# Kernel tuning notes

Measured on AMD Instinct MI355X. Metric: run time of the kernel, lower is better.

Reference implementation:

```python
import jax, jax.numpy as jnp
import numpy as np

B = 16384        # batch
P = 8            # num policies (experts)
D = 512          # latent dim
A = 64           # action dim
H = 1024         # hidden dim


def setup_inputs() -> dict:
    key = jax.random.key(0)
    ks = jax.random.split(key, 7)
    latents = jax.random.normal(ks[0], (B, D), dtype=jnp.float32)
    actions = jax.random.normal(ks[1], (B, A), dtype=jnp.float32)
    policy_indices = jax.random.randint(ks[2], (B,), 0, P, dtype=jnp.int64)
    # Per-policy 2-layer MLP params: concat(latent, action) -> hidden -> latent
    scale1 = 1.0 / np.sqrt(D + A)
    scale2 = 1.0 / np.sqrt(H)
    W1 = jax.random.normal(ks[3], (P, D + A, H), dtype=jnp.float32) * scale1
    b1 = jnp.zeros((P, H), dtype=jnp.float32)
    W2 = jax.random.normal(ks[4], (P, H, D), dtype=jnp.float32) * scale2
    b2 = jnp.zeros((P, D), dtype=jnp.float32)
    return {"latents": latents, "actions": actions, "policy_indices": policy_indices,
            "W1": W1, "b1": b1, "W2": W2, "b2": b2}


def reference(latents, actions, policy_indices, W1, b1, W2, b2):
    # Original: for each policy i, route rows with policy_indices == i through
    # that policy's dynamics model; scatter results back into next_latents.
    # Equivalent dense form: run all experts, then select per-row expert output.
    x = jnp.concatenate([latents, actions], axis=-1)          # [B, D+A]
    h = jax.nn.relu(jnp.einsum('bd,pdh->bph', x, W1) + b1)    # [B, P, H]
    y = jnp.einsum('bph,phd->bpd', h, W2) + b2                # [B, P, D]
    idx = policy_indices[:, None, None]                       # [B, 1, 1]
    next_latents = jnp.take_along_axis(y, idx, axis=1)[:, 0]  # [B, D]
    return next_latents
```

## Files before the change

kernel.cpp:

```cpp
#include <hip/hip_runtime.h>
#include <hip/hip_bf16.h>
#include <stdint.h>
#include <utility>

#define B_SZ 16384
#define P_SZ 8
#define D_SZ 512
#define A_SZ 64
#define K1 576
#define H_SZ 1024
#define NSEG 64
#define MB_MAX 264
#define BPAD (B_SZ + P_SZ*64)
#define PREP_BLOCKS (BPAD * 72 / 256)
#define TRANS_BLOCKS (32 * 32 * 16)

#define WAIT_VM8  0x0F78
#define WAIT_VM0  0x0F70

typedef __bf16 bf16_t;
typedef __bf16 bf16x8 __attribute__((ext_vector_type(8)));
typedef float f32x4 __attribute__((ext_vector_type(4)));

__device__ __forceinline__ void glds16(const void* g, void* l) {
    __builtin_amdgcn_global_load_lds(
        (const __attribute__((address_space(1))) unsigned*)g,
        (__attribute__((address_space(3))) unsigned*)l, 16, 0, 0);
}

template <int... Ks, typename F>
__device__ __forceinline__ void static_for_impl(std::integer_sequence<int, Ks...>, F&& f) {
    (f(std::integral_constant<int, Ks>{}), ...);
}
template <int N, typename F>
__device__ __forceinline__ void static_for(F&& f) {
    static_for_impl(std::make_integer_sequence<int, N>{}, (F&&)f);
}


__global__ __launch_bounds__(256) void hist_block(const int* __restrict__ pol,
                                                  int* __restrict__ blockhist,
                                                  int* __restrict__ rowidx) {
    __shared__ int lc[P_SZ];
    int t = threadIdx.x;
    if (t < P_SZ) lc[t] = 0;
    __syncthreads();
    int gid = blockIdx.x * 256 + t;
    rowidx[gid] = -1;
    if (gid < BPAD - B_SZ) rowidx[B_SZ + gid] = -1;
    atomicAdd(&lc[pol[gid]], 1);
    __syncthreads();
    if (t < P_SZ) blockhist[blockIdx.x * P_SZ + t] = lc[t];
}

__global__ __launch_bounds__(64) void prefix_kernel(const int* __restrict__ blockhist,
                                                    int* __restrict__ counts,
                                                    int* __restrict__ cursors,
                                                    int* __restrict__ blk_p) {
    int t = threadIdx.x;
    if (t < P_SZ) {
        int s = 0;
        for (int b = 0; b < NSEG; ++b) s += blockhist[b * P_SZ + t];
        counts[t] = s;
    }
    __syncthreads();
    if (t == 0) {
        int run = 0;
        for (int p = 0; p < P_SZ; ++p) {
            cursors[p] = run;
            int nb = (counts[p] + 63) >> 6;
            for (int b = 0; b < nb; ++b) blk_p[(run >> 6) + b] = p;
            run += nb * 64;
        }
        for (int b = run >> 6; b < MB_MAX; ++b) blk_p[b] = -1;
    }
}

__global__ __launch_bounds__(256) void scatter_agg(const int* __restrict__ pol,
                                                   int* __restrict__ cursors,
                                                   int* __restrict__ rowidx) {
    __shared__ int lc[P_SZ], base_s[P_SZ];
    int t = threadIdx.x;
    if (t < P_SZ) lc[t] = 0;
    __syncthreads();
    int i = blockIdx.x * 256 + t;
    int p = pol[i];
    int lpos = atomicAdd(&lc[p], 1);
    __syncthreads();
    if (t < P_SZ) base_s[t] = atomicAdd(&cursors[t], lc[t]);
    __syncthreads();
    rowidx[base_s[p] + lpos] = i;
}


__global__ __launch_bounds__(256) void prep_all(const float* __restrict__ latents,
                                                const float* __restrict__ actions,
                                                const int* __restrict__ rowidx,
                                                const float* __restrict__ W1,
                                                const float* __restrict__ W2,
                                                bf16_t* __restrict__ xs,
                                                bf16_t* __restrict__ w1t,
                                                bf16_t* __restrict__ w2t) {
    int bx = blockIdx.x;
    int tid = threadIdx.x;
    if (bx < PREP_BLOCKS) {
        int idx = bx * 256 + tid;
        int s = idx / 72;
        int col = (idx - s * 72) * 8;
        int g = rowidx[s];
        bf16x8 o;
        if (g < 0) {
            o = (bf16x8){0,0,0,0,0,0,0,0};
        } else {
            const float* src;
            if (col < D_SZ) src = latents + (size_t)g * D_SZ + col;
            else            src = actions + (size_t)g * A_SZ + (col - D_SZ);
            f32x4 v0 = *(const f32x4*)src;
            f32x4 v1 = *(const f32x4*)(src + 4);
            o[0] = (bf16_t)v0[0]; o[1] = (bf16_t)v0[1]; o[2] = (bf16_t)v0[2]; o[3] = (bf16_t)v0[3];
            o[4] = (bf16_t)v1[0]; o[5] = (bf16_t)v1[1]; o[6] = (bf16_t)v1[2]; o[7] = (bf16_t)v1[3];
        }
        *(bf16x8*)(xs + (size_t)s * K1 + col) = o;
        return;
    }
    int tz = bx - PREP_BLOCKS;
    int z = tz >> 10;
    int rem = tz & 1023;
    int k0 = (rem & 31) * 32, n0 = (rem >> 5) * 32;
    int K = (z < P_SZ) ? K1 : H_SZ;
    int N = (z < P_SZ) ? H_SZ : D_SZ;
    if (k0 >= K || n0 >= N) return;
    int p = z & 7;
    const float* Wp = ((z < P_SZ) ? W1 : W2) + (size_t)p * K * N;
    bf16_t* WTp = ((z < P_SZ) ? w1t : w2t) + (size_t)p * N * K;
    __shared__ float ls[32][33];
#pragma unroll
    for (int e = 0; e < 4; ++e) {
        int idx = e * 256 + tid;
        int kk = idx >> 5, nn = idx & 31;
        ls[kk][nn] = Wp[(size_t)(k0 + kk) * N + n0 + nn];
    }
    __syncthreads();
#pragma unroll
    for (int e = 0; e < 2; ++e) {
        int idx = e * 256 + tid;
        int nn = idx >> 4, kp = (idx & 15) * 2;
        union { bf16_t h[2]; unsigned u; } pk;
        pk.h[0] = (bf16_t)ls[kp][nn];
        pk.h[1] = (bf16_t)ls[kp + 1][nn];
        *(unsigned*)&WTp[(size_t)(n0 + nn) * K + k0 + kp] = pk.u;
    }
}


__global__ __launch_bounds__(64) void gemm1_kernel(
    const bf16_t* __restrict__ xs, const bf16_t* __restrict__ w1t,
    const float* __restrict__ b1, const int* __restrict__ blk_p,
    bf16_t* __restrict__ h) {

    const int p = blk_p[blockIdx.x];
    if (p < 0) return;
    const int m0 = blockIdx.x * 64;
    const int n0 = blockIdx.y * 64;

    __shared__ __align__(16) bf16_t As[3][64 * 32];
    __shared__ __align__(16) bf16_t Bs[3][64 * 32];

    const int lane = threadIdx.x;
    const bf16_t* a_src[4];
    const bf16_t* b_src[4];
    int dstc[4];
#pragma unroll
    for (int i = 0; i < 4; ++i) {
        int c = i * 64 + lane;
        int r = c >> 2;
        int kl = (c & 3) ^ ((r >> 1) & 3);
        a_src[i] = xs + (size_t)(m0 + r) * K1 + kl * 8;
        b_src[i] = w1t + ((size_t)p * H_SZ + n0 + r) * K1 + kl * 8;
        dstc[i] = c * 8;
    }

    const int l16 = lane & 15, qd = lane >> 4;
    const int swz = (l16 >> 1) & 3;
    int aoff[4], boff[4];
#pragma unroll
    for (int i = 0; i < 4; ++i) aoff[i] = (i * 16 + l16) * 32 + ((qd ^ swz) * 8);
#pragma unroll
    for (int j = 0; j < 4; ++j) boff[j] = (j * 16 + l16) * 32 + ((qd ^ swz) * 8);

    f32x4 acc[4][4];
#pragma unroll
    for (int i = 0; i < 4; ++i)
#pragma unroll
        for (int j = 0; j < 4; ++j)
            acc[i][j] = (f32x4){0.f, 0.f, 0.f, 0.f};

    constexpr int NK = K1 / 32;
#pragma unroll
    for (int i = 0; i < 4; ++i) glds16(a_src[i], &As[0][dstc[i]]);
#pragma unroll
    for (int i = 0; i < 4; ++i) glds16(b_src[i], &Bs[0][dstc[i]]);
#pragma unroll
    for (int i = 0; i < 4; ++i) glds16(a_src[i] + 32, &As[1][dstc[i]]);
#pragma unroll
    for (int i = 0; i < 4; ++i) glds16(b_src[i] + 32, &Bs[1][dstc[i]]);

    static_for<NK>([&](auto kc) {
        constexpr int k = kc.value;
        constexpr int cur = k % 3;
        if constexpr (k == NK - 1) __builtin_amdgcn_s_waitcnt(WAIT_VM0);
        else                       __builtin_amdgcn_s_waitcnt(WAIT_VM8);
        __builtin_amdgcn_sched_barrier(0);
        bf16x8 af[4], bfv[4];
#pragma unroll
        for (int i = 0; i < 4; ++i) af[i] = *(const bf16x8*)(&As[cur][aoff[i]]);
#pragma unroll
        for (int j = 0; j < 4; ++j) bfv[j] = *(const bf16x8*)(&Bs[cur][boff[j]]);
        if constexpr (k + 2 < NK) {
            constexpr int nxt = (k + 2) % 3;
#pragma unroll
            for (int i = 0; i < 4; ++i) glds16(a_src[i] + (k + 2) * 32, &As[nxt][dstc[i]]);
#pragma unroll
            for (int i = 0; i < 4; ++i) glds16(b_src[i] + (k + 2) * 32, &Bs[nxt][dstc[i]]);
        }
#pragma unroll
        for (int i = 0; i < 4; ++i)
#pragma unroll
            for (int j = 0; j < 4; ++j)
                acc[i][j] = __builtin_amdgcn_mfma_f32_16x16x32_bf16(af[i], bfv[j], acc[i][j], 0, 0, 0);
    });

#pragma unroll
    for (int i = 0; i < 4; ++i) {
#pragma unroll
        for (int r = 0; r < 4; ++r) {
            int ml = i * 16 + qd * 4 + r;
            size_t row = (size_t)(m0 + ml);
#pragma unroll
            for (int j = 0; j < 4; ++j) {
                int n = n0 + j * 16 + l16;
                float v = acc[i][j][r] + b1[p * H_SZ + n];
                h[row * H_SZ + n] = (bf16_t)fmaxf(v, 0.f);
            }
        }
    }
}

__global__ __launch_bounds__(64) void gemm2_kernel(
    const bf16_t* __restrict__ h, const bf16_t* __restrict__ w2t,
    const float* __restrict__ b2, const int* __restrict__ blk_p,
    const int* __restrict__ rowidx, float* __restrict__ out) {

    const int p = blk_p[blockIdx.x];
    if (p < 0) return;
    const int m0 = blockIdx.x * 64;
    const int n0 = blockIdx.y * 64;

    __shared__ __align__(16) bf16_t As[3][64 * 32];
    __shared__ __align__(16) bf16_t Bs[3][64 * 32];

    const int lane = threadIdx.x;
    const bf16_t* a_src[4];
    const bf16_t* b_src[4];
    int dstc[4];
#pragma unroll
    for (int i = 0; i < 4; ++i) {
        int c = i * 64 + lane;
        int r = c >> 2;
        int kl = (c & 3) ^ ((r >> 1) & 3);
        a_src[i] = h + (size_t)(m0 + r) * H_SZ + kl * 8;
        b_src[i] = w2t + ((size_t)p * D_SZ + n0 + r) * H_SZ + kl * 8;
        dstc[i] = c * 8;
    }

    const int l16 = lane & 15, qd = lane >> 4;
    const int swz = (l16 >> 1) & 3;
    int aoff[4], boff[4];
#pragma unroll
    for (int i = 0; i < 4; ++i) aoff[i] = (i * 16 + l16) * 32 + ((qd ^ swz) * 8);
#pragma unroll
    for (int j = 0; j < 4; ++j) boff[j] = (j * 16 + l16) * 32 + ((qd ^ swz) * 8);

    f32x4 acc[4][4];
#pragma unroll
    for (int i = 0; i < 4; ++i)
#pragma unroll
        for (int j = 0; j < 4; ++j)
            acc[i][j] = (f32x4){0.f, 0.f, 0.f, 0.f};

    constexpr int NK = H_SZ / 32;
#pragma unroll
    for (int i = 0; i < 4; ++i) glds16(a_src[i], &As[0][dstc[i]]);
#pragma unroll
    for (int i = 0; i < 4; ++i) glds16(b_src[i], &Bs[0][dstc[i]]);
#pragma unroll
    for (int i = 0; i < 4; ++i) glds16(a_src[i] + 32, &As[1][dstc[i]]);
#pragma unroll
    for (int i = 0; i < 4; ++i) glds16(b_src[i] + 32, &Bs[1][dstc[i]]);

    static_for<NK>([&](auto kc) {
        constexpr int k = kc.value;
        constexpr int cur = k % 3;
        if constexpr (k == NK - 1) __builtin_amdgcn_s_waitcnt(WAIT_VM0);
        else                       __builtin_amdgcn_s_waitcnt(WAIT_VM8);
        __builtin_amdgcn_sched_barrier(0);
        bf16x8 af[4], bfv[4];
#pragma unroll
        for (int i = 0; i < 4; ++i) af[i] = *(const bf16x8*)(&As[cur][aoff[i]]);
#pragma unroll
        for (int j = 0; j < 4; ++j) bfv[j] = *(const bf16x8*)(&Bs[cur][boff[j]]);
        if constexpr (k + 2 < NK) {
            constexpr int nxt = (k + 2) % 3;
#pragma unroll
            for (int i = 0; i < 4; ++i) glds16(a_src[i] + (k + 2) * 32, &As[nxt][dstc[i]]);
#pragma unroll
            for (int i = 0; i < 4; ++i) glds16(b_src[i] + (k + 2) * 32, &Bs[nxt][dstc[i]]);
        }
#pragma unroll
        for (int i = 0; i < 4; ++i)
#pragma unroll
            for (int j = 0; j < 4; ++j)
                acc[i][j] = __builtin_amdgcn_mfma_f32_16x16x32_bf16(af[i], bfv[j], acc[i][j], 0, 0, 0);
    });

#pragma unroll
    for (int i = 0; i < 4; ++i) {
#pragma unroll
        for (int r = 0; r < 4; ++r) {
            int ml = i * 16 + qd * 4 + r;
            int g = rowidx[m0 + ml];
            if (g >= 0) {
                size_t orow = (size_t)g * D_SZ;
#pragma unroll
                for (int j = 0; j < 4; ++j) {
                    int n = n0 + j * 16 + l16;
                    out[orow + n] = acc[i][j][r] + b2[p * D_SZ + n];
                }
            }
        }
    }
}


extern "C" void kernel_launch(void* const* d_in, const int* in_sizes, int n_in,
                              void* d_out, int out_size, void* d_ws, size_t ws_size,
                              hipStream_t stream) {
    const float* latents = (const float*)d_in[0];
    const float* actions = (const float*)d_in[1];
    const int*   pol     = (const int*)d_in[2];
    const float* W1      = (const float*)d_in[3];
    const float* b1      = (const float*)d_in[4];
    const float* W2      = (const float*)d_in[5];
    const float* b2      = (const float*)d_in[6];
    float* out = (float*)d_out;

    char* ws = (char*)d_ws;
    int* counts    = (int*)ws;
    int* cursors   = counts + P_SZ;
    int* blk_p     = cursors + P_SZ;
    int* blockhist = blk_p + MB_MAX;
    int* rowidx    = blockhist + NSEG * P_SZ;
    size_t pos = ((size_t)(2 * P_SZ + MB_MAX + NSEG * P_SZ + BPAD) * sizeof(int) + 255) & ~(size_t)255;
    bf16_t* xs  = (bf16_t*)(ws + pos);  pos += (size_t)BPAD * K1 * 2;
    bf16_t* hbuf= (bf16_t*)(ws + pos);  pos += (size_t)BPAD * H_SZ * 2;
    bf16_t* w1t = (bf16_t*)(ws + pos);  pos += (size_t)P_SZ * H_SZ * K1 * 2;
    bf16_t* w2t = (bf16_t*)(ws + pos);  pos += (size_t)P_SZ * D_SZ * H_SZ * 2;

    hist_block<<<NSEG, 256, 0, stream>>>(pol, blockhist, rowidx);
    prefix_kernel<<<1, 64, 0, stream>>>(blockhist, counts, cursors, blk_p);
    scatter_agg<<<NSEG, 256, 0, stream>>>(pol, cursors, rowidx);
    prep_all<<<PREP_BLOCKS + TRANS_BLOCKS, 256, 0, stream>>>(
        latents, actions, rowidx, W1, W2, xs, w1t, w2t);
    gemm1_kernel<<<dim3(MB_MAX, H_SZ / 64), 64, 0, stream>>>(xs, w1t, b1, blk_p, hbuf);
    gemm2_kernel<<<dim3(MB_MAX, D_SZ / 64), 64, 0, stream>>>(hbuf, w2t, b2, blk_p, rowidx, out);
}
```

Before: 238.1 us.

## Use 256-thread blocks with larger 256-row tiles in grouped GEMMs

Both expert GEMM kernels move from single-wave 64x64 tiles to four-wave blocks with 256-row M tiles (256x128 for the first GEMM, 256x64 for the second). Per-expert padding changes from 64 to 256 rows, and the block map and workspace sizes change to match. The goal is more reuse of each weight tile across rows and fewer blocks. In exchange, the triple-buffered async-load pipeline is replaced by a single buffer guarded by two barriers per K step, so loads no longer overlap compute, and more padded rows are computed.

Result: faster. 210.5 us (-11.6%).

```diff
diff --git a/kernel.cpp b/kernel.cpp
--- a/kernel.cpp
+++ b/kernel.cpp
@@ -1,7 +1,6 @@
 #include <hip/hip_runtime.h>
 #include <hip/hip_bf16.h>
 #include <stdint.h>
-#include <utility>
 
 #define B_SZ 16384
 #define P_SZ 8
@@ -10,13 +9,10 @@
 #define K1 576
 #define H_SZ 1024
 #define NSEG 64
-#define MB_MAX 264
-#define BPAD (B_SZ + P_SZ*64)
+#define MB_MAX 72
+#define BPAD (B_SZ + P_SZ*256)
 #define PREP_BLOCKS (BPAD * 72 / 256)
 #define TRANS_BLOCKS (32 * 32 * 16)
-
-#define WAIT_VM8  0x0F78
-#define WAIT_VM0  0x0F70
 
 typedef __bf16 bf16_t;
 typedef __bf16 bf16x8 __attribute__((ext_vector_type(8)));
@@ -26,15 +22,6 @@
     __builtin_amdgcn_global_load_lds(
         (const __attribute__((address_space(1))) unsigned*)g,
         (__attribute__((address_space(3))) unsigned*)l, 16, 0, 0);
-}
-
-template <int... Ks, typename F>
-__device__ __forceinline__ void static_for_impl(std::integer_sequence<int, Ks...>, F&& f) {
-    (f(std::integral_constant<int, Ks>{}), ...);
-}
-template <int N, typename F>
-__device__ __forceinline__ void static_for(F&& f) {
-    static_for_impl(std::make_integer_sequence<int, N>{}, (F&&)f);
 }
 
 
@@ -68,11 +55,11 @@
         int run = 0;
         for (int p = 0; p < P_SZ; ++p) {
             cursors[p] = run;
-            int nb = (counts[p] + 63) >> 6;
-            for (int b = 0; b < nb; ++b) blk_p[(run >> 6) + b] = p;
-            run += nb * 64;
+            int nb = (counts[p] + 255) >> 8;
+            for (int b = 0; b < nb; ++b) blk_p[(run >> 8) + b] = p;
+            run += nb * 256;
         }
-        for (int b = run >> 6; b < MB_MAX; ++b) blk_p[b] = -1;
+        for (int b = run >> 8; b < MB_MAX; ++b) blk_p[b] = -1;
     }
 }
 
@@ -153,91 +140,83 @@
 }
 
 
-__global__ __launch_bounds__(64) void gemm1_kernel(
+__global__ __launch_bounds__(256, 2) void gemm1_kernel(
     const bf16_t* __restrict__ xs, const bf16_t* __restrict__ w1t,
     const float* __restrict__ b1, const int* __restrict__ blk_p,
     bf16_t* __restrict__ h) {
 
     const int p = blk_p[blockIdx.x];
     if (p < 0) return;
-    const int m0 = blockIdx.x * 64;
-    const int n0 = blockIdx.y * 64;
-
-    __shared__ __align__(16) bf16_t As[3][64 * 32];
-    __shared__ __align__(16) bf16_t Bs[3][64 * 32];
-
-    const int lane = threadIdx.x;
-    const bf16_t* a_src[4];
-    const bf16_t* b_src[4];
-    int dstc[4];
+    const int m0 = blockIdx.x * 256;
+    const int n0 = blockIdx.y * 128;
+
+    __shared__ __align__(16) bf16_t As[256 * 32];
+    __shared__ __align__(16) bf16_t Bs[128 * 32];
+
+    const int tid = threadIdx.x;
+    const int wave = tid >> 6, lane = tid & 63;
+
+    const bf16_t* a_src[4]; bf16_t* a_dst[4];
 #pragma unroll
     for (int i = 0; i < 4; ++i) {
-        int c = i * 64 + lane;
+        int c = (wave * 4 + i) * 64 + lane;
         int r = c >> 2;
         int kl = (c & 3) ^ ((r >> 1) & 3);
         a_src[i] = xs + (size_t)(m0 + r) * K1 + kl * 8;
+        a_dst[i] = As + c * 8;
+    }
+    const bf16_t* b_src[2]; bf16_t* b_dst[2];
+#pragma unroll
+    for (int i = 0; i < 2; ++i) {
+        int c = (wave * 2 + i) * 64 + lane;
+        int r = c >> 2;
+        int kl = (c & 3) ^ ((r >> 1) & 3);
         b_src[i] = w1t + ((size_t)p * H_SZ + n0 + r) * K1 + kl * 8;
-        dstc[i] = c * 8;
+        b_dst[i] = Bs + c * 8;
     }
 
     const int l16 = lane & 15, qd = lane >> 4;
     const int swz = (l16 >> 1) & 3;
-    int aoff[4], boff[4];
-#pragma unroll
-    for (int i = 0; i < 4; ++i) aoff[i] = (i * 16 + l16) * 32 + ((qd ^ swz) * 8);
-#pragma unroll
-    for (int j = 0; j < 4; ++j) boff[j] = (j * 16 + l16) * 32 + ((qd ^ swz) * 8);
-
-    f32x4 acc[4][4];
+    int aoff[4], boff[8];
+#pragma unroll
+    for (int i = 0; i < 4; ++i) aoff[i] = (wave * 64 + i * 16 + l16) * 32 + ((qd ^ swz) * 8);
+#pragma unroll
+    for (int j = 0; j < 8; ++j) boff[j] = (j * 16 + l16) * 32 + ((qd ^ swz) * 8);
+
+    f32x4 acc[4][8];
 #pragma unroll
     for (int i = 0; i < 4; ++i)
 #pragma unroll
-        for (int j = 0; j < 4; ++j)
+        for (int j = 0; j < 8; ++j)
             acc[i][j] = (f32x4){0.f, 0.f, 0.f, 0.f};
 
-    constexpr int NK = K1 / 32;
-#pragma unroll
-    for (int i = 0; i < 4; ++i) glds16(a_src[i], &As[0][dstc[i]]);
-#pragma unroll
-    for (int i = 0; i < 4; ++i) glds16(b_src[i], &Bs[0][dstc[i]]);
-#pragma unroll
-    for (int i = 0; i < 4; ++i) glds16(a_src[i] + 32, &As[1][dstc[i]]);
-#pragma unroll
-    for (int i = 0; i < 4; ++i) glds16(b_src[i] + 32, &Bs[1][dstc[i]]);
-
-    static_for<NK>([&](auto kc) {
-        constexpr int k = kc.value;
-        constexpr int cur = k % 3;
-        if constexpr (k == NK - 1) __builtin_amdgcn_s_waitcnt(WAIT_VM0);
-        else                       __builtin_amdgcn_s_waitcnt(WAIT_VM8);
-        __builtin_amdgcn_sched_barrier(0);
-        bf16x8 af[4], bfv[4];
-#pragma unroll
-        for (int i = 0; i < 4; ++i) af[i] = *(const bf16x8*)(&As[cur][aoff[i]]);
-#pragma unroll
-        for (int j = 0; j < 4; ++j) bfv[j] = *(const bf16x8*)(&Bs[cur][boff[j]]);
-        if constexpr (k + 2 < NK) {
-            constexpr int nxt = (k + 2) % 3;
-#pragma unroll
-            for (int i = 0; i < 4; ++i) glds16(a_src[i] + (k + 2) * 32, &As[nxt][dstc[i]]);
-#pragma unroll
-            for (int i = 0; i < 4; ++i) glds16(b_src[i] + (k + 2) * 32, &Bs[nxt][dstc[i]]);
-        }
+    for (int kt = 0; kt < K1; kt += 32) {
+        __syncthreads();
+#pragma unroll
+        for (int i = 0; i < 4; ++i) glds16(a_src[i] + kt, a_dst[i]);
+#pragma unroll
+        for (int i = 0; i < 2; ++i) glds16(b_src[i] + kt, b_dst[i]);
+        __syncthreads();
+        bf16x8 af[4], bfv[8];
+#pragma unroll
+        for (int i = 0; i < 4; ++i) af[i] = *(const bf16x8*)(As + aoff[i]);
+#pragma unroll
+        for (int j = 0; j < 8; ++j) bfv[j] = *(const bf16x8*)(Bs + boff[j]);
 #pragma unroll
         for (int i = 0; i < 4; ++i)
 #pragma unroll
-            for (int j = 0; j < 4; ++j)
+            for (int j = 0; j < 8; ++j)
                 acc[i][j] = __builtin_amdgcn_mfma_f32_16x16x32_bf16(af[i], bfv[j], acc[i][j], 0, 0, 0);
-    });
+    }
 
 #pragma unroll
     for (int i = 0; i < 4; ++i) {
 #pragma unroll
         for (int r = 0; r < 4; ++r) {
-            int ml = i * 16 + qd * 4 + r;
+            int ml = wave * 64 + i * 16 + qd * 4 + r;
             size_t row = (size_t)(m0 + ml);
 #pragma unroll
-            for (int j = 0; j < 4; ++j) {
+            for (int j = 0; j < 8; ++j) {
                 int n = n0 + j * 16 + l16;
                 float v = acc[i][j][r] + b1[p * H_SZ + n];
                 h[row * H_SZ + n] = (bf16_t)fmaxf(v, 0.f);
@@ -246,38 +225,45 @@
     }
 }
 
-__global__ __launch_bounds__(64) void gemm2_kernel(
+__global__ __launch_bounds__(256, 2) void gemm2_kernel(
     const bf16_t* __restrict__ h, const bf16_t* __restrict__ w2t,
     const float* __restrict__ b2, const int* __restrict__ blk_p,
     const int* __restrict__ rowidx, float* __restrict__ out) {
 
     const int p = blk_p[blockIdx.x];
     if (p < 0) return;
-    const int m0 = blockIdx.x * 64;
+    const int m0 = blockIdx.x * 256;
     const int n0 = blockIdx.y * 64;
 
-    __shared__ __align__(16) bf16_t As[3][64 * 32];
-    __shared__ __align__(16) bf16_t Bs[3][64 * 32];
-
-    const int lane = threadIdx.x;
-    const bf16_t* a_src[4];
-    const bf16_t* b_src[4];
-    int dstc[4];
+    __shared__ __align__(16) bf16_t As[256 * 32];
+    __shared__ __align__(16) bf16_t Bs[64 * 32];
+
+    const int tid = threadIdx.x;
+    const int wave = tid >> 6, lane = tid & 63;
+
+    const bf16_t* a_src[4]; bf16_t* a_dst[4];
 #pragma unroll
     for (int i = 0; i < 4; ++i) {
-        int c = i * 64 + lane;
+        int c = (wave * 4 + i) * 64 + lane;
         int r = c >> 2;
         int kl = (c & 3) ^ ((r >> 1) & 3);
         a_src[i] = h + (size_t)(m0 + r) * H_SZ + kl * 8;
-        b_src[i] = w2t + ((size_t)p * D_SZ + n0 + r) * H_SZ + kl * 8;
-        dstc[i] = c * 8;
+        a_dst[i] = As + c * 8;
+    }
+    const bf16_t* b_src0; bf16_t* b_dst0;
+    {
+        int c = wave * 64 + lane;
+        int r = c >> 2;
+        int kl = (c & 3) ^ ((r >> 1) & 3);
+        b_src0 = w2t + ((size_t)p * D_SZ + n0 + r) * H_SZ + kl * 8;
+        b_dst0 = Bs + c * 8;
     }
 
     const int l16 = lane & 15, qd = lane >> 4;
     const int swz = (l16 >> 1) & 3;
     int aoff[4], boff[4];
 #pragma unroll
-    for (int i = 0; i < 4; ++i) aoff[i] = (i * 16 + l16) * 32 + ((qd ^ swz) * 8);
+    for (int i = 0; i < 4; ++i) aoff[i] = (wave * 64 + i * 16 + l16) * 32 + ((qd ^ swz) * 8);
 #pragma unroll
     for (int j = 0; j < 4; ++j) boff[j] = (j * 16 + l16) * 32 + ((qd ^ swz) * 8);
 
@@ -288,46 +274,29 @@
         for (int j = 0; j < 4; ++j)
             acc[i][j] = (f32x4){0.f, 0.f, 0.f, 0.f};
 
-    constexpr int NK = H_SZ / 32;
-#pragma unroll
-    for (int i = 0; i < 4; ++i) glds16(a_src[i], &As[0][dstc[i]]);
-#pragma unroll
-    for (int i = 0; i < 4; ++i) glds16(b_src[i], &Bs[0][dstc[i]]);
-#pragma unroll
-    for (int i = 0; i < 4; ++i) glds16(a_src[i] + 32, &As[1][dstc[i]]);
-#pragma unroll
-    for (int i = 0; i < 4; ++i) glds16(b_src[i] + 32, &Bs[1][dstc[i]]);
-
-    static_for<NK>([&](auto kc) {
-        constexpr int k = kc.value;
-        constexpr int cur = k % 3;
-        if constexpr (k == NK - 1) __builtin_amdgcn_s_waitcnt(WAIT_VM0);
-        else                       __builtin_amdgcn_s_waitcnt(WAIT_VM8);
-        __builtin_amdgcn_sched_barrier(0);
+    for (int kt = 0; kt < H_SZ; kt += 32) {
+        __syncthreads();
+#pragma unroll
+        for (int i = 0; i < 4; ++i) glds16(a_src[i] + kt, a_dst[i]);
+        glds16(b_src0 + kt, b_dst0);
+        __syncthreads();
         bf16x8 af[4], bfv[4];
 #pragma unroll
-        for (int i = 0; i < 4; ++i) af[i] = *(const bf16x8*)(&As[cur][aoff[i]]);
-#pragma unroll
-        for (int j = 0; j < 4; ++j) bfv[j] = *(const bf16x8*)(&Bs[cur][boff[j]]);
-        if constexpr (k + 2 < NK) {
-            constexpr int nxt = (k + 2) % 3;
-#pragma unroll
-            for (int i = 0; i < 4; ++i) glds16(a_src[i] + (k + 2) * 32, &As[nxt][dstc[i]]);
-#pragma unroll
-            for (int i = 0; i < 4; ++i) glds16(b_src[i] + (k + 2) * 32, &Bs[nxt][dstc[i]]);
-        }
+        for (int i = 0; i < 4; ++i) af[i] = *(const bf16x8*)(As + aoff[i]);
+#pragma unroll
+        for (int j = 0; j < 4; ++j) bfv[j] = *(const bf16x8*)(Bs + boff[j]);
 #pragma unroll
         for (int i = 0; i < 4; ++i)
 #pragma unroll
             for (int j = 0; j < 4; ++j)
                 acc[i][j] = __builtin_amdgcn_mfma_f32_16x16x32_bf16(af[i], bfv[j], acc[i][j], 0, 0, 0);
-    });
+    }
 
 #pragma unroll
     for (int i = 0; i < 4; ++i) {
 #pragma unroll
         for (int r = 0; r < 4; ++r) {
-            int ml = i * 16 + qd * 4 + r;
+            int ml = wave * 64 + i * 16 + qd * 4 + r;
             int g = rowidx[m0 + ml];
             if (g >= 0) {
                 size_t orow = (size_t)g * D_SZ;
@@ -371,6 +340,6 @@
     scatter_agg<<<NSEG, 256, 0, stream>>>(pol, cursors, rowidx);
     prep_all<<<PREP_BLOCKS + TRANS_BLOCKS, 256, 0, stream>>>(
         latents, actions, rowidx, W1, W2, xs, w1t, w2t);
-    gemm1_kernel<<<dim3(MB_MAX, H_SZ / 64), 64, 0, stream>>>(xs, w1t, b1, blk_p, hbuf);
-    gemm2_kernel<<<dim3(MB_MAX, D_SZ / 64), 64, 0, stream>>>(hbuf, w2t, b2, blk_p, rowidx, out);
-}
+    gemm1_kernel<<<dim3(MB_MAX, H_SZ / 128), 256, 0, stream>>>(xs, w1t, b1, blk_p, hbuf);
+    gemm2_kernel<<<dim3(MB_MAX, D_SZ / 64), 256, 0, stream>>>(hbuf, w2t, b2, blk_p, rowidx, out);
+}
```
